# Performance work log

Hardware: AMD Instinct MI355X
Metric: run time of the kernel (lower is better)

Reference implementation:

```python
import jax, jax.numpy as jnp
import numpy as np

NEG_SLOPE = 0.2  # PyG GATConv default negative_slope


def gat_conv(x, edge_index, W, att_src, att_dst, bias):
    # PyG GATConv, heads=1, add_self_loops=True, lin bias=False, final bias added
    N = x.shape[0]
    h = x @ W                                     # [N, F]
    loops = jnp.arange(N, dtype=edge_index.dtype)
    src = jnp.concatenate([edge_index[0], loops])
    dst = jnp.concatenate([edge_index[1], loops])
    a_src = h @ att_src                           # [N]
    a_dst = h @ att_dst                           # [N]
    e = a_src[src] + a_dst[dst]
    e = jnp.where(e > 0, e, NEG_SLOPE * e)        # leaky_relu
    m = jax.ops.segment_max(e, dst, num_segments=N)
    w = jnp.exp(e - m[dst])
    denom = jax.ops.segment_sum(w, dst, num_segments=N)
    alpha = w / denom[dst]
    out = jax.ops.segment_sum(h[src] * alpha[:, None], dst, num_segments=N)
    return out + bias


def gcn_conv(x, edge_index, W, b):
    # PyG GCNConv: add self-loops + symmetric normalization
    N = x.shape[0]
    loops = jnp.arange(N, dtype=edge_index.dtype)
    src = jnp.concatenate([edge_index[0], loops])
    dst = jnp.concatenate([edge_index[1], loops])
    deg = jax.ops.segment_sum(jnp.ones(src.shape[0], dtype=x.dtype), dst, num_segments=N)
    dinv = jax.lax.rsqrt(jnp.maximum(deg, 1e-12))  # deg >= 1 thanks to self-loops
    norm = dinv[src] * dinv[dst]
    xw = x @ W
    return jax.ops.segment_sum(xw[src] * norm[:, None], dst, num_segments=N) + b


def get_final_node(x, batch, num_graphs):
    nn_ = jax.ops.segment_sum(jnp.ones(x.shape[0], dtype=jnp.int32), batch, num_segments=num_graphs)
    cum = jnp.concatenate([jnp.zeros(1, dtype=nn_.dtype), jnp.cumsum(nn_)[:-1]])
    return x[cum]


def ontology_emb(table, e1, e2, W, asrc, adst, b, idx_map):
    emb = gat_conv(table, e1, W, asrc, adst, b)
    emb = gat_conv(emb, e2, W, asrc, adst, b)
    return emb[idx_map]


def _forward(spec_emb, diag_table, proce_table, atc_table,
             diag_W, diag_asrc, diag_adst, diag_b,
             proce_W, proce_asrc, proce_adst, proce_b,
             atc_W, atc_asrc, atc_adst, atc_b,
             gcn_W1, gcn_b1, gcn_W2, gcn_b2, gcn_W3, gcn_b3,
             diag_e1, diag_e2, proce_e1, proce_e2, atc_e1, atc_e2,
             diag_map, proce_map, atc_map,
             left_x, left_graph_index, right_x, right_graph_index,
             left_x_batch, right_x_batch, num_graphs):
    diag_emb = ontology_emb(diag_table, diag_e1, diag_e2, diag_W, diag_asrc, diag_adst, diag_b, diag_map)
    proce_emb = ontology_emb(proce_table, proce_e1, proce_e2, proce_W, proce_asrc, proce_adst, proce_b, proce_map)
    atc_emb = ontology_emb(atc_table, atc_e1, atc_e2, atc_W, atc_asrc, atc_adst, atc_b, atc_map)
    all_emb = jnp.concatenate([spec_emb, diag_emb, proce_emb, atc_emb], axis=0)
    lh = all_emb[left_x[:, 0]]   # squeeze(dim=1)
    rh = all_emb[right_x[:, 0]]
    for W, b in ((gcn_W1, gcn_b1), (gcn_W2, gcn_b2), (gcn_W3, gcn_b3)):
        lh = gcn_conv(lh, left_graph_index, W, b)
        rh = gcn_conv(rh, right_graph_index, W, b)
    lf = get_final_node(lh, left_x_batch, num_graphs)
    rf = get_final_node(rh, right_x_batch, num_graphs)
    eps = 1e-6  # CosineSimilarity eps
    num = jnp.sum(lf * rf, axis=-1)
    den = jnp.maximum(jnp.linalg.norm(lf, axis=-1), eps) * jnp.maximum(jnp.linalg.norm(rf, axis=-1), eps)
    return num / den


def setup_inputs() -> dict:
    key = jax.random.key(0)
    ks = jax.random.split(key, 32)
    HID = 128
    B, NPG = 2048, 50
    N = B * NPG               # 102400 nodes per side
    E_PAT = 409600            # 4 edges per node
    DIAG_N, DIAG_L = 30000, 20000
    PROCE_N, PROCE_L = 12000, 8000
    ATC_N, ATC_L = 6000, 4000
    ALL = 1 + DIAG_L + PROCE_L + ATC_L
    f = lambda k, s: jax.random.normal(k, s, dtype=jnp.float32)
    scale = 0.1
    inp = {
        'spec_emb': f(ks[0], (1, HID)),
        'diag_table': f(ks[1], (DIAG_N, HID)),
        'proce_table': f(ks[2], (PROCE_N, HID)),
        'atc_table': f(ks[3], (ATC_N, HID)),
    }
    for i, nm in enumerate(['diag', 'proce', 'atc']):
        inp[nm + '_W'] = f(ks[4 + i], (HID, HID)) * scale
        inp[nm + '_asrc'] = f(ks[7 + i], (HID,)) * scale
        inp[nm + '_adst'] = f(ks[10 + i], (HID,)) * scale
        inp[nm + '_b'] = jnp.zeros((HID,), jnp.float32)
    for j in range(3):
        inp['gcn_W%d' % (j + 1)] = f(ks[13 + j], (HID, HID)) * scale
        inp['gcn_b%d' % (j + 1)] = jnp.zeros((HID,), jnp.float32)
    inp['diag_e1'] = jax.random.randint(ks[16], (2, DIAG_N), 0, DIAG_N, dtype=jnp.int32)
    inp['diag_e2'] = jax.random.randint(ks[17], (2, DIAG_N), 0, DIAG_N, dtype=jnp.int32)
    inp['proce_e1'] = jax.random.randint(ks[18], (2, PROCE_N), 0, PROCE_N, dtype=jnp.int32)
    inp['proce_e2'] = jax.random.randint(ks[19], (2, PROCE_N), 0, PROCE_N, dtype=jnp.int32)
    inp['atc_e1'] = jax.random.randint(ks[20], (2, ATC_N), 0, ATC_N, dtype=jnp.int32)
    inp['atc_e2'] = jax.random.randint(ks[21], (2, ATC_N), 0, ATC_N, dtype=jnp.int32)
    inp['diag_map'] = jnp.arange(DIAG_L, dtype=jnp.int32)
    inp['proce_map'] = jnp.arange(PROCE_L, dtype=jnp.int32)
    inp['atc_map'] = jnp.arange(ATC_L, dtype=jnp.int32)
    inp['left_x'] = jax.random.randint(ks[22], (N, 1), 0, ALL, dtype=jnp.int32)
    inp['right_x'] = jax.random.randint(ks[23], (N, 1), 0, ALL, dtype=jnp.int32)
    inp['left_graph_index'] = jax.random.randint(ks[24], (2, E_PAT), 0, N, dtype=jnp.int32)
    inp['right_graph_index'] = jax.random.randint(ks[25], (2, E_PAT), 0, N, dtype=jnp.int32)
    batch = jnp.repeat(jnp.arange(B, dtype=jnp.int32), NPG)
    inp['left_x_batch'] = batch
    inp['right_x_batch'] = batch
    inp['num_graphs'] = B
    return inp


def reference(spec_emb, diag_table, proce_table, atc_table,
              diag_W, diag_asrc, diag_adst, diag_b,
              proce_W, proce_asrc, proce_adst, proce_b,
              atc_W, atc_asrc, atc_adst, atc_b,
              gcn_W1, gcn_b1, gcn_W2, gcn_b2, gcn_W3, gcn_b3,
              diag_e1, diag_e2, proce_e1, proce_e2, atc_e1, atc_e2,
              diag_map, proce_map, atc_map,
              left_x, left_graph_index, right_x, right_graph_index,
              left_x_batch, right_x_batch, num_graphs):
    return _forward(spec_emb, diag_table, proce_table, atc_table,
                    diag_W, diag_asrc, diag_adst, diag_b,
                    proce_W, proce_asrc, proce_adst, proce_b,
                    atc_W, atc_asrc, atc_adst, atc_b,
                    gcn_W1, gcn_b1, gcn_W2, gcn_b2, gcn_W3, gcn_b3,
                    diag_e1, diag_e2, proce_e1, proce_e2, atc_e1, atc_e2,
                    diag_map, proce_map, atc_map,
                    left_x, left_graph_index, right_x, right_graph_index,
                    left_x_batch, right_x_batch, num_graphs)
```

## Files before the change

kernel.cpp:

```cpp
#include <hip/hip_runtime.h>
#include <hip/hip_bf16.h>

#define HID 128

typedef unsigned int uint;
typedef unsigned short ushort;
typedef short short8 __attribute__((ext_vector_type(8)));
typedef float f32x4 __attribute__((ext_vector_type(4)));

static inline int cdiv_i(long a, long b) { return (int)((a + b - 1) / b); }

__device__ __forceinline__ float bf2f(uint hi) {
    return __builtin_bit_cast(float, hi << 16);
}
__device__ __forceinline__ ushort f2bf(float f) {
    uint u = __builtin_bit_cast(uint, f);
    u = (u + 0x7fffu + ((u >> 16) & 1u)) >> 16;
    return (ushort)u;
}

__global__ void fold1(const float* __restrict__ W2, const float* __restrict__ b2,
                      const float* __restrict__ W3, float* __restrict__ W23b) {
    const int idx = blockIdx.x * 256 + threadIdx.x;
    if (idx >= 129 * 128) return;
    const int i = idx >> 7, j = idx & 127;
    const float* a = (i < 128) ? (W2 + i * 128) : b2;
    float s = 0.f;
#pragma unroll 8
    for (int k = 0; k < 128; ++k) s += a[k] * W3[k * 128 + j];
    W23b[idx] = s;
}

__global__ void fold2(const float* __restrict__ W1, const float* __restrict__ b1,
                      const float* __restrict__ W23b, float* __restrict__ Pout) {
    const int idx = blockIdx.x * 256 + threadIdx.x;
    if (idx >= 130 * 128) return;
    const int i = idx >> 7, j = idx & 127;
    if (i == 129) { Pout[idx] = W23b[128 * 128 + j]; return; }
    const float* a = (i < 128) ? (W1 + i * 128) : b1;
    float s = 0.f;
#pragma unroll 8
    for (int k = 0; k < 128; ++k) s += a[k] * W23b[k * 128 + j];
    Pout[idx] = s;
}

struct W4 { const float* w[4]; };

__global__ void wtrans_k(W4 ws, ushort* __restrict__ out) {
    const int idx = blockIdx.x * 256 + threadIdx.x;
    if (idx >= 4 * 16384) return;
    const int m = idx >> 14;
    const int e = idx & 16383;
    const int n = e >> 7, k = e & 127;
    out[idx] = f2bf(ws.w[m][k * 128 + n]);
}

__device__ __forceinline__ void stage_wt(const ushort* __restrict__ Wt,
                                         ushort* __restrict__ wl) {
    const int t = threadIdx.x;
    const int row = t >> 1, half = (t & 1) * 64;
    const uint4* src = (const uint4*)(Wt + row * 128 + half);
    uint4* dst = (uint4*)(wl + row * 136 + half);
#pragma unroll
    for (int i = 0; i < 8; ++i) dst[i] = src[i];
}

template <typename AT>
__device__ __forceinline__ void load_afrag(const AT* __restrict__ A, long row,
                                           int koff, short8& af) {
    if constexpr (__is_same(AT, ushort)) {
        const uint4 raw = *(const uint4*)(A + row * 128 + koff);
        af = __builtin_bit_cast(short8, raw);
    } else {
        const float4* p = (const float4*)(A + row * 128 + koff);
        const float4 x0 = p[0], x1 = p[1];
        af[0] = (short)f2bf(x0.x); af[1] = (short)f2bf(x0.y);
        af[2] = (short)f2bf(x0.z); af[3] = (short)f2bf(x0.w);
        af[4] = (short)f2bf(x1.x); af[5] = (short)f2bf(x1.y);
        af[6] = (short)f2bf(x1.z); af[7] = (short)f2bf(x1.w);
    }
}

template <typename AT, typename OT>
__device__ __forceinline__ void mfma_tile(const AT* __restrict__ A,
                                          const ushort* __restrict__ wl,
                                          const float* __restrict__ bias,
                                          OT* __restrict__ C,
                                          long m0blk, long rowEnd) {
    const int tid = threadIdx.x;
    const int wave = tid >> 6, lane = tid & 63;
    const int r = lane & 15, q = lane >> 4;
    const long m0 = m0blk + wave * 32;

    f32x4 acc[2][8];
#pragma unroll
    for (int mi = 0; mi < 2; ++mi)
#pragma unroll
        for (int ni = 0; ni < 8; ++ni) acc[mi][ni] = (f32x4)0.f;

#pragma unroll
    for (int t = 0; t < 4; ++t) {
        const int koff = t * 32 + q * 8;
        short8 bfr[8];
#pragma unroll
        for (int ni = 0; ni < 8; ++ni) {
            const uint4 raw = *(const uint4*)(&wl[(ni * 16 + r) * 136 + koff]);
            bfr[ni] = __builtin_bit_cast(short8, raw);
        }
#pragma unroll
        for (int mi = 0; mi < 2; ++mi) {
            long row = m0 + mi * 16 + r;
            if (row >= rowEnd) row = rowEnd - 1;
            short8 af;
            load_afrag<AT>(A, row, koff, af);
#pragma unroll
            for (int ni = 0; ni < 8; ++ni)
                acc[mi][ni] = __builtin_amdgcn_mfma_f32_16x16x32_bf16(
                    af, bfr[ni], acc[mi][ni], 0, 0, 0);
        }
    }

#pragma unroll
    for (int mi = 0; mi < 2; ++mi) {
#pragma unroll
        for (int ni = 0; ni < 8; ++ni) {
            const int col = ni * 16 + r;
            const float bv = bias ? bias[col] : 0.f;
#pragma unroll
            for (int reg = 0; reg < 4; ++reg) {
                const long row = m0 + mi * 16 + q * 4 + reg;
                if (row < rowEnd) {
                    const float v = acc[mi][ni][reg] + bv;
                    if constexpr (__is_same(OT, ushort))
                        C[row * 128 + col] = f2bf(v);
                    else
                        C[row * 128 + col] = v;
                }
            }
        }
    }
}

template <typename OT>
__global__ __launch_bounds__(256) void gemm_gcn(const ushort* __restrict__ A,
                                                const ushort* __restrict__ Wt,
                                                const float* __restrict__ bias,
                                                OT* __restrict__ C, int M) {
    __shared__ ushort wl[128 * 136];
    stage_wt(Wt, wl);
    __syncthreads();
    const long m0 = (long)blockIdx.x * 256;
    mfma_tile<ushort, OT>(A, wl, bias, C, m0, M);
    if (m0 + 128 < M)
        mfma_tile<ushort, OT>(A, wl, bias, C, m0 + 128, M);
}

struct GOnto {
    const ushort* Wt0; const ushort* Wt1; const ushort* Wt2;
    const float* s0; const float* s1; const float* s2;
    const float* d0; const float* d1; const float* d2;
    int bs1, bs2;
    int r1, r2, r3;
};

template <typename AT>
__global__ __launch_bounds__(256) void gemm_onto(const AT* x0, const AT* x1,
                                                 const AT* x2, GOnto g,
                                                 ushort* __restrict__ H,
                                                 float* __restrict__ as_o,
                                                 float* __restrict__ ad_o) {
    __shared__ ushort wl[128 * 136];
    const int b = blockIdx.x;
    const int gid = (b >= g.bs1) + (b >= g.bs2);
    const ushort* Wt = (gid == 0) ? g.Wt0 : (gid == 1) ? g.Wt1 : g.Wt2;
    const float* avs = (gid == 0) ? g.s0 : (gid == 1) ? g.s1 : g.s2;
    const float* avd = (gid == 0) ? g.d0 : (gid == 1) ? g.d1 : g.d2;
    const AT* Ag = (gid == 0) ? x0 : (gid == 1) ? x1 : x2;
    const int bloc = b - ((gid == 0) ? 0 : (gid == 1) ? g.bs1 : g.bs2);
    const long rb = (gid == 0) ? 0 : (gid == 1) ? g.r1 : g.r2;
    const long Mg = ((gid == 0) ? g.r1 : (gid == 1) ? g.r2 : g.r3) - rb;
    stage_wt(Wt, wl);
    __syncthreads();

    const int tid = threadIdx.x;
    const int wave = tid >> 6, lane = tid & 63;
    const int r = lane & 15, q = lane >> 4;
    const long m0 = (long)bloc * 128 + wave * 32;

    f32x4 acc[2][8];
#pragma unroll
    for (int mi = 0; mi < 2; ++mi)
#pragma unroll
        for (int ni = 0; ni < 8; ++ni) acc[mi][ni] = (f32x4)0.f;

#pragma unroll
// ... 39 lines not shown
        adv[ni] = avd[ni * 16 + r];
    }
#pragma unroll
    for (int mi = 0; mi < 2; ++mi) {
#pragma unroll
        for (int reg = 0; reg < 4; ++reg) {
            float ps = 0.f, pd = 0.f;
#pragma unroll
            for (int ni = 0; ni < 8; ++ni) {
                ps += acc[mi][ni][reg] * asv[ni];
                pd += acc[mi][ni][reg] * adv[ni];
            }
#pragma unroll
            for (int o = 1; o < 16; o <<= 1) {
                ps += __shfl_xor(ps, o);
                pd += __shfl_xor(pd, o);
            }
            const long row = m0 + mi * 16 + q * 4 + reg;
            if (r == 0 && row < Mg) {
                as_o[rb + row] = ps;
                ad_o[rb + row] = pd;
            }
        }
    }
}

struct GatP {
    int r1, r2;
    int ob0, ob1, ob2;
    const float* b0; const float* b1; const float* b2;
};

__device__ __forceinline__ void acc8(float* acc, float w, const uint4 v) {
    acc[0] += w * bf2f(v.x & 0xffff);
    acc[1] += w * bf2f(v.x >> 16);
    acc[2] += w * bf2f(v.y & 0xffff);
    acc[3] += w * bf2f(v.y >> 16);
    acc[4] += w * bf2f(v.z & 0xffff);
    acc[5] += w * bf2f(v.z >> 16);
    acc[6] += w * bf2f(v.w & 0xffff);
    acc[7] += w * bf2f(v.w >> 16);
}

__global__ __launch_bounds__(256) void gat_all(const ushort* __restrict__ h,
                                               const float* __restrict__ as,
                                               const float* __restrict__ ad,
// ... 28 lines not shown
        const uint4 v0 = *(const uint4*)(h + (size_t)(rb + s0) * 128 + ql * 8);
        const uint4 v1 = *(const uint4*)(h + (size_t)(rb + s1) * 128 + ql * 8);
        denom += w0 + w1;
        acc8(acc, w0, v0);
        acc8(acc, w1, v1);
    }
    if (j < end) {
        const int s0 = srcl[j];
        float e0 = as[rb + s0] + adv; e0 = (e0 > 0.f) ? e0 : 0.2f * e0;
        const float w0 = __expf(e0 - m);
        const uint4 v0 = *(const uint4*)(h + (size_t)(rb + s0) * 128 + ql * 8);
        denom += w0;
        acc8(acc, w0, v0);
    }
    const float inv = 1.f / denom;
    const float4 bv0 = *(const float4*)(bias + ql * 8);
    const float4 bv1 = *(const float4*)(bias + ql * 8 + 4);
    uint4 o;
    o.x = (uint)f2bf(acc[0] * inv + bv0.x) | ((uint)f2bf(acc[1] * inv + bv0.y) << 16);
    o.y = (uint)f2bf(acc[2] * inv + bv0.z) | ((uint)f2bf(acc[3] * inv + bv0.w) << 16);
    o.z = (uint)f2bf(acc[4] * inv + bv1.x) | ((uint)f2bf(acc[5] * inv + bv1.y) << 16);
    o.w = (uint)f2bf(acc[6] * inv + bv1.z) | ((uint)f2bf(acc[7] * inv + bv1.w) << 16);
    *(uint4*)(out + (size_t)node * 128 + ql * 8) = o;
}

struct CsrDesc {
    const int* esrc[8];
    const int* edst[8];
    int ebase[9];
    int nbase[9];
    int totE;
};

__global__ void csr_count_b(CsrDesc d, int* __restrict__ cnt, int* __restrict__ pos) {
    const int i = blockIdx.x * 256 + threadIdx.x;
    if (i >= d.totE) return;
    int li = 0;
#pragma unroll
    for (int k = 1; k < 8; ++k) li += (i >= d.ebase[k]);
    const int v = d.nbase[li] + d.edst[li][i - d.ebase[li]];
    pos[i] = atomicAdd(&cnt[v], 1);
}

__global__ void csr_fill_b(CsrDesc d, const int* __restrict__ offs,
                           const int* __restrict__ pos, const int* __restrict__ cnt,
                           int* __restrict__ srcl, int4* __restrict__ pedge,
                           const float* __restrict__ dinv,
                           const int* __restrict__ lx, const int* __restrict__ rx,
                           const int* __restrict__ mk,
                           int NP, int NV, int pB) {
    const int i = blockIdx.x * 256 + threadIdx.x;
    int v, s, li, idx;
    if (i < d.totE) {
        li = 0;
#pragma unroll
        for (int k = 1; k < 8; ++k) li += (i >= d.ebase[k]);
        const int j = i - d.ebase[li];
        v = d.nbase[li] + d.edst[li][j];
        s = d.esrc[li][j];
        idx = offs[v] + pos[i];
    } else if (i < d.totE + NV) {
        v = i - d.totE;
        li = 0;
#pragma unroll
        for (int k = 1; k < 8; ++k) li += (v >= d.nbase[k]);
        s = v - d.nbase[li];
        idx = offs[v] + cnt[v];
    } else return;
    if (li >= 6) {
        const int n2l = v - d.nbase[6];
        if (mk[n2l] == 0) return;
        const int sg = (li - 6) * NP + s;
        int4 rec;
        rec.x = sg;
        rec.y = (li == 7 ? rx : lx)[s];
        rec.z = __float_as_int(dinv[n2l] * dinv[sg]);
        rec.w = 0;
        pedge[idx - pB] = rec;
    } else {
        srcl[idx] = s;
    }
}

__global__ void first_node(const int* __restrict__ bL, const int* __restrict__ bR,
                           int NP, int* __restrict__ gfL, int* __restrict__ gfR,
                           int* __restrict__ mk) {
    const int i = blockIdx.x * 256 + threadIdx.x;
    if (i >= 2 * NP) return;
    const int side = i >= NP;
    const int ii = i - (side ? NP : 0);
    const int* b = side ? bR : bL;
    int* gf = side ? gfR : gfL;
    const int cur = b[ii];
    const int prev = (ii == 0) ? -1 : b[ii - 1];
    if (cur > prev) {
        for (int g = prev + 1; g <= cur; ++g) gf[g] = ii;
        mk[i] = 1;
    }
}

__global__ void mark_k(const int* __restrict__ lEg, const int* __restrict__ rEg,
                       int EP, int NP, int* __restrict__ mk, int testBit, int setBit) {
    const int i = blockIdx.x * 256 + threadIdx.x;
    int src, dst;
    if (i < 2 * EP) {
        const int side = i >= EP;
        const int e = i - side * EP;
        const int* eg = side ? rEg : lEg;
        src = side * NP + eg[e];
        dst = side * NP + eg[EP + e];
    } else if (i < 2 * EP + 2 * NP) {
        src = dst = i - 2 * EP;
    } else return;
    if (mk[dst] & testBit) atomicOr(&mk[src], setBit);
}

__global__ __launch_bounds__(1024) void scan_tile(const int* __restrict__ in,
                                                  int* __restrict__ out,
                                                  int* __restrict__ bsum, int n,
                                                  int pn0, int pcnt,
                                                  float* __restrict__ dinv) {
    __shared__ int buf[1024];
    const int tid = threadIdx.x;
    const int i = blockIdx.x * 1024 + tid;
    const int v = (i < n) ? (in[i] + 1) : 0;
    if (i >= pn0 && i < pn0 + pcnt)
        dinv[i - pn0] = rsqrtf(fmaxf((float)v, 1e-12f));
    buf[tid] = v;
    __syncthreads();
    int x = v;
    for (int o = 1; o < 1024; o <<= 1) {
        const int t = (tid >= o) ? buf[tid - o] : 0;
        __syncthreads();
        x += t;
        buf[tid] = x;
        __syncthreads();
    }
    if (i < n) out[i] = x - v;
    if (tid == 1023) bsum[blockIdx.x] = x;
}

__global__ __launch_bounds__(1024) void scan_single(int* __restrict__ bsum, int nb) {
    __shared__ int buf[1024];
    const int tid = threadIdx.x;
    const int v = (tid < nb) ? bsum[tid] : 0;
    buf[tid] = v;
    __syncthreads();
    int x = v;
    for (int o = 1; o < 1024; o <<= 1) {
        const int t = (tid >= o) ? buf[tid - o] : 0;
        __syncthreads();
        x += t;
        buf[tid] = x;
        __syncthreads();
    }
    if (tid < nb) bsum[tid] = x - v;
    if (tid == 1023) bsum[nb] = x;
}

__global__ void scan_add(int* __restrict__ out, const int* __restrict__ bsum,
                         int n, int nb) {
    const int i = blockIdx.x * 256 + threadIdx.x;
    if (i < n) out[i] += bsum[i >> 10];
    else if (i == n) out[i] = bsum[nb];
}

struct EmbD {
    const float* spec; const ushort* oE;
    const int* m0; const int* m1; const int* m2;
    int lb2, lb3;
    int r1, r2;
    long ALLr;
};

__global__ void build_emb(EmbD d, ushort* __restrict__ out) {
    const long t = (long)blockIdx.x * 256 + threadIdx.x;
    if (t >= d.ALLr * 16) return;
    const int row = (int)(t >> 4), c = (int)(t & 15);
    uint4 o;
    if (row == 0) {
        const float4 f0 = ((const float4*)d.spec)[c * 2];
        const float4 f1 = ((const float4*)d.spec)[c * 2 + 1];
        o.x = (uint)f2bf(f0.x) | ((uint)f2bf(f0.y) << 16);
        o.y = (uint)f2bf(f0.z) | ((uint)f2bf(f0.w) << 16);
        o.z = (uint)f2bf(f1.x) | ((uint)f2bf(f1.y) << 16);
        o.w = (uint)f2bf(f1.z) | ((uint)f2bf(f1.w) << 16);
    } else {
        const int seg = (row >= d.lb2) + (row >= d.lb3);
        const int local = row - ((seg == 0) ? 1 : (seg == 1) ? d.lb2 : d.lb3);
        const int* mp = (seg == 0) ? d.m0 : (seg == 1) ? d.m1 : d.m2;
        const int rb = (seg == 0) ? 0 : (seg == 1) ? d.r1 : d.r2;
        o = ((const uint4*)(d.oE + (size_t)(rb + mp[local]) * 128))[c];
    }
    ((uint4*)out)[(size_t)row * 16 + c] = o;
}

__global__ __launch_bounds__(256) void gcn_agg1(const ushort* __restrict__ A3,
                                                const int4* __restrict__ pedge,
                                                const int* __restrict__ offs6,
                                                const float* __restrict__ c1,
                                                ushort* __restrict__ t1,
                                                const int* __restrict__ mk,
                                                int NP2, int pB) {
    const int n2 = blockIdx.x * 16 + (threadIdx.x >> 4);
    const int ql = threadIdx.x & 15;
    if (n2 >= NP2) return;
    if ((mk[n2] & 4) == 0) return;
    const int beg = offs6[n2] - pB, end = offs6[n2 + 1] - pB;
    float acc[8] = {0.f, 0.f, 0.f, 0.f, 0.f, 0.f, 0.f, 0.f};
    int j = beg;
    for (; j + 2 <= end; j += 2) {
        const int4 r0 = pedge[j], r1 = pedge[j + 1];
        const float w0 = __int_as_float(r0.z), w1 = __int_as_float(r1.z);
        const uint4 v0 = *(const uint4*)(A3 + (size_t)r0.y * 128 + ql * 8);
        const uint4 v1 = *(const uint4*)(A3 + (size_t)r1.y * 128 + ql * 8);
        acc8(acc, w0, v0);
        acc8(acc, w1, v1);
// ... 145 lines not shown
    int nb_acc = 0;
    for (int i = 0; i < 8; ++i) {
        dsc.ebase[i + 1] = dsc.ebase[i] + eCnt[i];
        dsc.nbase[i] = nb_acc;
        nb_acc += nCnt[i];
    }
    const int NV = nb_acc;
    dsc.nbase[8] = NV;
    dsc.totE = dsc.ebase[8];
    const int totEntries = dsc.totE + NV;
    const int pB = dsc.ebase[6] + dsc.nbase[6];
    const int pEntries = totEntries - pB;

    char* ws = (char*)d_ws;
    size_t off = 0;
    auto alloc = [&](size_t bytes) -> void* {
        off = (off + 255) & ~(size_t)255;
        void* p = ws + off;
        off += bytes;
        return p;
    };
    ushort* wt4 = (ushort*)alloc((size_t)4 * 16384 * 2);
    float* W23b = (float*)alloc((size_t)129 * 128 * 4);
    float* Pout = (float*)alloc((size_t)130 * 128 * 4);
    ushort* allemb = (ushort*)alloc((size_t)ALL * HID * 2);
    ushort* A3 = (ushort*)alloc((size_t)ALL * HID * 2);
    int* cnt = (int*)alloc((size_t)NV * 4);
    int* offs = (int*)alloc((size_t)(NV + 1) * 4);
    int* pos = (int*)alloc((size_t)dsc.totE * 4);
    int* srcl = (int*)alloc((size_t)pB * 4);
    int4* pedge = (int4*)alloc((size_t)pEntries * 16);
    int* bsum = (int*)alloc(1025 * 4);
    float* dinv = (float*)alloc((size_t)2 * NP * 4);
    float* as = (float*)alloc((size_t)Mtot * 4);
    float* ad = (float*)alloc((size_t)Mtot * 4);
    int* gfL = (int*)alloc((size_t)(B + 1) * 4);
    int* gfR = (int*)alloc((size_t)(B + 1) * 4);
    int* mk = (int*)alloc((size_t)2 * NP * 4);
    ushort* t1 = (ushort*)alloc((size_t)2 * NP * HID * 2);
    ushort* big = (ushort*)alloc((size_t)2 * NP * HID * 2);
    ushort* hbuf = big;
    ushort* obuf = big + (size_t)Mtot * HID;
    ushort* t2 = big;

    fold1<<<cdiv_i(129 * 128, 256), 256, 0, stream>>>(gcnW[1], gcnB[1], gcnW[2], W23b);
    fold2<<<cdiv_i(130 * 128, 256), 256, 0, stream>>>(gcnW[0], gcnB[0], W23b, Pout);
    const float* c1 = Pout + 128 * 128;
    const float* c2 = Pout + 129 * 128;

    W4 w4;
    w4.w[0] = ontW[0]; w4.w[1] = ontW[1]; w4.w[2] = ontW[2]; w4.w[3] = Pout;
    wtrans_k<<<cdiv_i(4 * 16384, 256), 256, 0, stream>>>(w4, wt4);
    const ushort* wtOnt[3] = {wt4, wt4 + 16384, wt4 + 2 * 16384};
    const ushort* WpT = wt4 + 3 * 16384;

    hipMemsetAsync(mk, 0, (size_t)2 * NP * 4, stream);
    first_node<<<cdiv_i(2 * NP, 256), 256, 0, stream>>>(left_batch, right_batch,
                                                        NP, gfL, gfR, mk);
    mark_k<<<cdiv_i(2 * EP + 2 * NP, 256), 256, 0, stream>>>(
        left_eg, right_eg, EP, NP, mk, 1, 2);
    mark_k<<<cdiv_i(2 * EP + 2 * NP, 256), 256, 0, stream>>>(
        left_eg, right_eg, EP, NP, mk, 2, 4);

    hipMemsetAsync(cnt, 0, (size_t)NV * 4, stream);
    csr_count_b<<<cdiv_i(dsc.totE, 256), 256, 0, stream>>>(dsc, cnt, pos);
    {
        const int nb = cdiv_i(NV, 1024);
        scan_tile<<<nb, 1024, 0, stream>>>(cnt, offs, bsum, NV, dsc.nbase[6],
                                           2 * NP, dinv);
        scan_single<<<1, 1024, 0, stream>>>(bsum, nb);
        scan_add<<<cdiv_i(NV + 1, 256), 256, 0, stream>>>(offs, bsum, NV, nb);
    }
    csr_fill_b<<<cdiv_i(totEntries, 256), 256, 0, stream>>>(dsc, offs, pos, cnt,
                                                            srcl, pedge, dinv,
                                                            left_x, right_x, mk,
                                                            NP, NV, pB);

    GOnto go;
    go.Wt0 = wtOnt[0]; go.Wt1 = wtOnt[1]; go.Wt2 = wtOnt[2];
    go.s0 = ontAs[0]; go.s1 = ontAs[1]; go.s2 = ontAs[2];
    go.d0 = ontAd[0]; go.d1 = ontAd[1]; go.d2 = ontAd[2];
    go.bs1 = cdiv_i(Ms[0], 128);
    go.bs2 = go.bs1 + cdiv_i(Ms[1], 128);
    const int totBlk = go.bs2 + cdiv_i(Ms[2], 128);
    go.r1 = r1; go.r2 = r2; go.r3 = Mtot;

    for (int layer = 0; layer < 2; ++layer) {
        const GatP gp{r1, r2,
                      dsc.nbase[0 + layer], dsc.nbase[2 + layer], dsc.nbase[4 + layer],
                      ontB[0], ontB[1], ontB[2]};
        if (layer == 0)
            gemm_onto<float><<<totBlk, 256, 0, stream>>>(tabs[0], tabs[1], tabs[2],
                                                         go, hbuf, as, ad);
        else
            gemm_onto<ushort><<<totBlk, 256, 0, stream>>>(
                obuf, obuf + (size_t)r1 * HID, obuf + (size_t)r2 * HID,
                go, hbuf, as, ad);
        gat_all<<<cdiv_i(Mtot, 16), 256, 0, stream>>>(hbuf, as, ad, offs, srcl, gp,
                                                      obuf, Mtot);
    }

    EmbD ed;
    ed.spec = spec; ed.oE = obuf;
    ed.m0 = maps[0]; ed.m1 = maps[1]; ed.m2 = maps[2];
    ed.lb2 = 1 + Ls[0]; ed.lb3 = 1 + Ls[0] + Ls[1];
    ed.r1 = r1; ed.r2 = r2; ed.ALLr = ALL;
    build_emb<<<cdiv_i(ALL * 16, 256), 256, 0, stream>>>(ed, allemb);

    const int* offs6 = offs + dsc.nbase[6];
    gemm_gcn<ushort><<<cdiv_i(ALL, 256), 256, 0, stream>>>(
        allemb, WpT, nullptr, A3, (int)ALL);
    gcn_agg1<<<cdiv_i(2 * NP, 16), 256, 0, stream>>>(A3, pedge, offs6, c1, t1,
                                                     mk, 2 * NP, pB);
    gcn_agg2<<<cdiv_i(2 * NP, 16), 256, 0, stream>>>(t1, pedge, offs6, c2, t2,
                                                     mk, 2 * NP, pB);
    final_cos<<<cdiv_i(B, 8), 256, 0, stream>>>(t2, pedge, offs6, gfL, gfR,
                                                gcnB[2], (float*)d_out, B, NP, pB);
}
```

Baseline: 396.1 us.

## Fuse preprocessing kernels into packed launches and gather embeddings inside GEMM

Independent setup kernels (weight folding, transposes, memsets, first-node, CSR count, mark passes, layer-1 GEMM) are merged into a few multi-role launches that dispatch on block index. The three-kernel scan becomes two kernels. The embedding build is folded into the patient GEMM's A-fragment load, and fold2 writes the transposed bf16 weight directly. This removes many launch gaps and an intermediate buffer round trip, at the cost of heterogeneous blocks sharing one launch and padding shared-memory use onto blocks that never need it.

```diff
diff --git a/kernel.cpp b/kernel.cpp
--- a/kernel.cpp
+++ b/kernel.cpp
@@ -9,6 +9,7 @@
 typedef float f32x4 __attribute__((ext_vector_type(4)));
 
 static inline int cdiv_i(long a, long b) { return (int)((a + b - 1) / b); }
+static inline int imax_i(int a, int b) { return a > b ? a : b; }
 
 __device__ __forceinline__ float bf2f(uint hi) {
     return __builtin_bit_cast(float, hi << 16);
@@ -19,41 +20,13 @@
     return (ushort)u;
 }
 
-__global__ void fold1(const float* __restrict__ W2, const float* __restrict__ b2,
-                      const float* __restrict__ W3, float* __restrict__ W23b) {
-    const int idx = blockIdx.x * 256 + threadIdx.x;
-    if (idx >= 129 * 128) return;
-    const int i = idx >> 7, j = idx & 127;
-    const float* a = (i < 128) ? (W2 + i * 128) : b2;
-    float s = 0.f;
-#pragma unroll 8
-    for (int k = 0; k < 128; ++k) s += a[k] * W3[k * 128 + j];
-    W23b[idx] = s;
-}
-
-__global__ void fold2(const float* __restrict__ W1, const float* __restrict__ b1,
-                      const float* __restrict__ W23b, float* __restrict__ Pout) {
-    const int idx = blockIdx.x * 256 + threadIdx.x;
-    if (idx >= 130 * 128) return;
-    const int i = idx >> 7, j = idx & 127;
-    if (i == 129) { Pout[idx] = W23b[128 * 128 + j]; return; }
-    const float* a = (i < 128) ? (W1 + i * 128) : b1;
-    float s = 0.f;
-#pragma unroll 8
-    for (int k = 0; k < 128; ++k) s += a[k] * W23b[k * 128 + j];
-    Pout[idx] = s;
-}
-
-struct W4 { const float* w[4]; };
-
-__global__ void wtrans_k(W4 ws, ushort* __restrict__ out) {
-    const int idx = blockIdx.x * 256 + threadIdx.x;
-    if (idx >= 4 * 16384) return;
-    const int m = idx >> 14;
-    const int e = idx & 16383;
-    const int n = e >> 7, k = e & 127;
-    out[idx] = f2bf(ws.w[m][k * 128 + n]);
-}
+struct CsrDesc {
+    const int* esrc[8];
+    const int* edst[8];
+    int ebase[9];
+    int nbase[9];
+    int totE;
+};
 
 __device__ __forceinline__ void stage_wt(const ushort* __restrict__ Wt,
                                          ushort* __restrict__ wl) {
@@ -81,80 +54,6 @@
     }
 }
 
-template <typename AT, typename OT>
-__device__ __forceinline__ void mfma_tile(const AT* __restrict__ A,
-                                          const ushort* __restrict__ wl,
-                                          const float* __restrict__ bias,
-                                          OT* __restrict__ C,
-                                          long m0blk, long rowEnd) {
-    const int tid = threadIdx.x;
-    const int wave = tid >> 6, lane = tid & 63;
-    const int r = lane & 15, q = lane >> 4;
-    const long m0 = m0blk + wave * 32;
-
-    f32x4 acc[2][8];
-#pragma unroll
-    for (int mi = 0; mi < 2; ++mi)
-#pragma unroll
-        for (int ni = 0; ni < 8; ++ni) acc[mi][ni] = (f32x4)0.f;
-
-#pragma unroll
-    for (int t = 0; t < 4; ++t) {
-        const int koff = t * 32 + q * 8;
-        short8 bfr[8];
-#pragma unroll
-        for (int ni = 0; ni < 8; ++ni) {
-            const uint4 raw = *(const uint4*)(&wl[(ni * 16 + r) * 136 + koff]);
-            bfr[ni] = __builtin_bit_cast(short8, raw);
-        }
-#pragma unroll
-        for (int mi = 0; mi < 2; ++mi) {
-            long row = m0 + mi * 16 + r;
-            if (row >= rowEnd) row = rowEnd - 1;
-            short8 af;
-            load_afrag<AT>(A, row, koff, af);
-#pragma unroll
-            for (int ni = 0; ni < 8; ++ni)
-                acc[mi][ni] = __builtin_amdgcn_mfma_f32_16x16x32_bf16(
-                    af, bfr[ni], acc[mi][ni], 0, 0, 0);
-        }
-    }
-
-#pragma unroll
-    for (int mi = 0; mi < 2; ++mi) {
-#pragma unroll
-        for (int ni = 0; ni < 8; ++ni) {
-            const int col = ni * 16 + r;
-            const float bv = bias ? bias[col] : 0.f;
-#pragma unroll
-            for (int reg = 0; reg < 4; ++reg) {
-                const long row = m0 + mi * 16 + q * 4 + reg;
-                if (row < rowEnd) {
-                    const float v = acc[mi][ni][reg] + bv;
-                    if constexpr (__is_same(OT, ushort))
-                        C[row * 128 + col] = f2bf(v);
-                    else
-                        C[row * 128 + col] = v;
-                }
-            }
-        }
-    }
-}
-
-template <typename OT>
-__global__ __launch_bounds__(256) void gemm_gcn(const ushort* __restrict__ A,
-                                                const ushort* __restrict__ Wt,
-                                                const float* __restrict__ bias,
-                                                OT* __restrict__ C, int M) {
-    __shared__ ushort wl[128 * 136];
-    stage_wt(Wt, wl);
-    __syncthreads();
-    const long m0 = (long)blockIdx.x * 256;
-    mfma_tile<ushort, OT>(A, wl, bias, C, m0, M);
-    if (m0 + 128 < M)
-        mfma_tile<ushort, OT>(A, wl, bias, C, m0 + 128, M);
-}
-
 struct GOnto {
     const ushort* Wt0; const ushort* Wt1; const ushort* Wt2;
     const float* s0; const float* s1; const float* s2;
@@ -164,13 +63,11 @@
 };
 
 template <typename AT>
-__global__ __launch_bounds__(256) void gemm_onto(const AT* x0, const AT* x1,
-                                                 const AT* x2, GOnto g,
-                                                 ushort* __restrict__ H,
-                                                 float* __restrict__ as_o,
-                                                 float* __restrict__ ad_o) {
-    __shared__ ushort wl[128 * 136];
-    const int b = blockIdx.x;
+__device__ void gemm_onto_dev(int b, const AT* __restrict__ x0,
+                              const AT* __restrict__ x1, const AT* __restrict__ x2,
+                              const GOnto& g, ushort* __restrict__ H,
+                              float* __restrict__ as_o, float* __restrict__ ad_o,
+                              ushort* __restrict__ wl) {
     const int gid = (b >= g.bs1) + (b >= g.bs2);
     const ushort* Wt = (gid == 0) ? g.Wt0 : (gid == 1) ? g.Wt1 : g.Wt2;
     const float* avs = (gid == 0) ? g.s0 : (gid == 1) ? g.s1 : g.s2;
@@ -256,6 +153,342 @@
                 ad_o[rb + row] = pd;
             }
         }
+    }
+}
+
+__global__ __launch_bounds__(256) void gemm_onto_l2(const ushort* __restrict__ x0,
+                                                    const ushort* __restrict__ x1,
+                                                    const ushort* __restrict__ x2,
+                                                    GOnto g, ushort* __restrict__ H,
+                                                    float* __restrict__ as_o,
+                                                    float* __restrict__ ad_o) {
+    __shared__ ushort wl[128 * 136];
+    gemm_onto_dev<ushort>(blockIdx.x, x0, x1, x2, g, H, as_o, ad_o, wl);
+}
+
+struct EmbSrc {
+    const float* spec; const ushort* oE;
+    const int* m0; const int* m1; const int* m2;
+    int lb2, lb3, r1, r2;
+};
+
+__device__ __forceinline__ short8 load_emb(const EmbSrc& e, long row, int koff) {
+    short8 af;
+    if (row == 0) {
+        const float4* pp = (const float4*)(e.spec + koff);
+        const float4 x0 = pp[0], x1 = pp[1];
+        af[0] = (short)f2bf(x0.x); af[1] = (short)f2bf(x0.y);
+        af[2] = (short)f2bf(x0.z); af[3] = (short)f2bf(x0.w);
+        af[4] = (short)f2bf(x1.x); af[5] = (short)f2bf(x1.y);
+        af[6] = (short)f2bf(x1.z); af[7] = (short)f2bf(x1.w);
+        return af;
+    }
+    const int r = (int)row;
+    const int seg = (r >= e.lb2) + (r >= e.lb3);
+    const int local = r - ((seg == 0) ? 1 : (seg == 1) ? e.lb2 : e.lb3);
+    const int* mp = (seg == 0) ? e.m0 : (seg == 1) ? e.m1 : e.m2;
+    const int rb = (seg == 0) ? 0 : (seg == 1) ? e.r1 : e.r2;
+    const long sr = (long)rb + mp[local];
+    return __builtin_bit_cast(short8, *(const uint4*)(e.oE + sr * 128 + koff));
+}
+
+__device__ void gemm_pat_tile(const EmbSrc& es, const ushort* __restrict__ wl,
+                              ushort* __restrict__ C, long m0blk, long rowEnd) {
+    const int tid = threadIdx.x;
+    const int wave = tid >> 6, lane = tid & 63;
+    const int r = lane & 15, q = lane >> 4;
+    const long m0 = m0blk + wave * 32;
+
+    f32x4 acc[2][8];
+#pragma unroll
+    for (int mi = 0; mi < 2; ++mi)
+#pragma unroll
+        for (int ni = 0; ni < 8; ++ni) acc[mi][ni] = (f32x4)0.f;
+
+#pragma unroll
+    for (int t = 0; t < 4; ++t) {
+        const int koff = t * 32 + q * 8;
+        short8 bfr[8];
+#pragma unroll
+        for (int ni = 0; ni < 8; ++ni) {
+            const uint4 raw = *(const uint4*)(&wl[(ni * 16 + r) * 136 + koff]);
+            bfr[ni] = __builtin_bit_cast(short8, raw);
+        }
+#pragma unroll
+        for (int mi = 0; mi < 2; ++mi) {
+            long row = m0 + mi * 16 + r;
+            if (row >= rowEnd) row = rowEnd - 1;
+            const short8 af = load_emb(es, row, koff);
+#pragma unroll
+            for (int ni = 0; ni < 8; ++ni)
+                acc[mi][ni] = __builtin_amdgcn_mfma_f32_16x16x32_bf16(
+                    af, bfr[ni], acc[mi][ni], 0, 0, 0);
+        }
+    }
+
+#pragma unroll
+    for (int mi = 0; mi < 2; ++mi) {
+#pragma unroll
+        for (int ni = 0; ni < 8; ++ni) {
+            const int col = ni * 16 + r;
+#pragma unroll
+            for (int reg = 0; reg < 4; ++reg) {
+                const long row = m0 + mi * 16 + q * 4 + reg;
+                if (row < rowEnd) C[row * 128 + col] = f2bf(acc[mi][ni][reg]);
+            }
+        }
+    }
+}
+
+__global__ __launch_bounds__(256) void gemm_pat(EmbSrc es,
+                                                const ushort* __restrict__ Wt,
+                                                ushort* __restrict__ C, int M) {
+    __shared__ ushort wl[128 * 136];
+    stage_wt(Wt, wl);
+    __syncthreads();
+    const long m0 = (long)blockIdx.x * 256;
+    gemm_pat_tile(es, wl, C, m0, M);
+    if (m0 + 128 < M) gemm_pat_tile(es, wl, C, m0 + 128, M);
+}
+
+__device__ __forceinline__ void fold1_dev(int idx, const float* __restrict__ W2,
+                                          const float* __restrict__ b2,
+                                          const float* __restrict__ W3,
+                                          float* __restrict__ W23b) {
+    if (idx >= 129 * 128) return;
+    const int i = idx >> 7, j = idx & 127;
+    const float* a = (i < 128) ? (W2 + i * 128) : b2;
+    float s = 0.f;
+#pragma unroll 8
+    for (int k = 0; k < 128; ++k) s += a[k] * W3[k * 128 + j];
+    W23b[idx] = s;
+}
+
+__device__ __forceinline__ void fold2_dev(int idx, const float* __restrict__ W1,
+                                          const float* __restrict__ b1,
+                                          const float* __restrict__ W23b,
+                                          ushort* __restrict__ WpT,
+                                          float* __restrict__ cbuf) {
+    if (idx >= 130 * 128) return;
+    const int i = idx >> 7, j = idx & 127;
+    if (i == 129) { cbuf[128 + j] = W23b[128 * 128 + j]; return; }
+    const float* a = (i < 128) ? (W1 + i * 128) : b1;
+    float s = 0.f;
+#pragma unroll 8
+    for (int k = 0; k < 128; ++k) s += a[k] * W23b[k * 128 + j];
+    if (i < 128) WpT[j * 128 + i] = f2bf(s);
+    else cbuf[j] = s;
+}
+
+__device__ __forceinline__ void mark_dev(int i, const int* __restrict__ lEg,
+                                         const int* __restrict__ rEg, int EP,
+                                         int NP, int* __restrict__ mk,
+                                         int testBit, int setBit) {
+    int src, dst;
+    if (i < 2 * EP) {
+        const int side = i >= EP;
+        const int e = i - side * EP;
+        const int* eg = side ? rEg : lEg;
+        src = side * NP + eg[e];
+        dst = side * NP + eg[EP + e];
+    } else if (i < 2 * EP + 2 * NP) {
+        src = dst = i - 2 * EP;
+    } else return;
+    if (mk[dst] & testBit) atomicOr(&mk[src], setBit);
+}
+
+__device__ __forceinline__ void csr_count_dev(int i, const CsrDesc& d,
+                                              int* __restrict__ cnt,
+                                              int* __restrict__ pos) {
+    if (i >= d.totE) return;
+    int li = 0;
+#pragma unroll
+    for (int k = 1; k < 8; ++k) li += (i >= d.ebase[k]);
+    const int v = d.nbase[li] + d.edst[li][i - d.ebase[li]];
+    pos[i] = atomicAdd(&cnt[v], 1);
+}
+
+struct PackPrep {
+    const float* W2; const float* b2; const float* W3; float* W23b;
+    const float* wsrc[3]; ushort* wt_out;
+    int* cnt; int NV;
+    const int* bL; const int* bR; int NP;
+    int* gfL; int* gfR; int* mk;
+    int nbF1, nbWT, nbInit;
+};
+
+__global__ __launch_bounds__(256) void k_prep(PackPrep p) {
+    const int b = blockIdx.x, tid = threadIdx.x;
+    if (b < p.nbF1) {
+        fold1_dev(b * 256 + tid, p.W2, p.b2, p.W3, p.W23b);
+    } else if (b < p.nbF1 + p.nbWT) {
+        const int idx = (b - p.nbF1) * 256 + tid;
+        if (idx < 3 * 16384) {
+            const int m = idx >> 14;
+            const int e = idx & 16383;
+            const int n = e >> 7, k = e & 127;
+            p.wt_out[idx] = f2bf(p.wsrc[m][k * 128 + n]);
+        }
+    } else {
+        const int i = (b - p.nbF1 - p.nbWT) * 256 + tid;
+        if (i < p.NV) p.cnt[i] = 0;
+        if (i < 2 * p.NP) {
+            const int side = i >= p.NP;
+            const int ii = i - (side ? p.NP : 0);
+            const int* bb = side ? p.bR : p.bL;
+            int* gf = side ? p.gfR : p.gfL;
+            const int cur = bb[ii];
+            const int prev = (ii == 0) ? -1 : bb[ii - 1];
+            int m = 0;
+            if (cur > prev) {
+                for (int g = prev + 1; g <= cur; ++g) gf[g] = ii;
+                m = 1;
+            }
+            p.mk[i] = m;
+        }
+    }
+}
+
+struct PackA {
+    const float* W1; const float* b1; const float* W23b;
+    ushort* WpT; float* cbuf;
+    CsrDesc dsc; int* cnt; int* pos;
+    const int* lEg; const int* rEg; int EP; int NP; int* mk;
+    const float* x0; const float* x1; const float* x2;
+    GOnto go; ushort* H; float* as_o; float* ad_o;
+    int nbF2, nbCnt, nbMark;
+};
+
+__global__ __launch_bounds__(256) void k_packA(PackA p) {
+    __shared__ ushort wl[128 * 136];
+    const int b = blockIdx.x, tid = threadIdx.x;
+    if (b < p.nbF2) {
+        fold2_dev(b * 256 + tid, p.W1, p.b1, p.W23b, p.WpT, p.cbuf);
+    } else if (b < p.nbF2 + p.nbCnt) {
+        csr_count_dev((b - p.nbF2) * 256 + tid, p.dsc, p.cnt, p.pos);
+    } else if (b < p.nbF2 + p.nbCnt + p.nbMark) {
+        mark_dev((b - p.nbF2 - p.nbCnt) * 256 + tid, p.lEg, p.rEg, p.EP, p.NP,
+                 p.mk, 1, 2);
+    } else {
+        gemm_onto_dev<float>(b - p.nbF2 - p.nbCnt - p.nbMark, p.x0, p.x1, p.x2,
+                             p.go, p.H, p.as_o, p.ad_o, wl);
+    }
+}
+
+struct PackB {
+    const int* cnt; int* offs; int* bsum;
+    int NV; int pn0; int pcnt; float* dinv;
+    const int* lEg; const int* rEg; int EP; int NP; int* mk;
+    int nbScan;
+};
+
+__device__ void scan_tile_dev(const int* __restrict__ in, int* __restrict__ out,
+                              int* __restrict__ bsum, int n, int pn0, int pcnt,
+                              float* __restrict__ dinv, int tb, int tid,
+                              int* sbuf) {
+    const int base = tb * 1024 + tid * 4;
+    int v[4];
+    int s = 0;
+#pragma unroll
+    for (int k = 0; k < 4; ++k) {
+        const int i = base + k;
+        v[k] = (i < n) ? (in[i] + 1) : 0;
+        if (i >= pn0 && i < pn0 + pcnt)
+            dinv[i - pn0] = rsqrtf(fmaxf((float)v[k], 1e-12f));
+        s += v[k];
+    }
+    sbuf[tid] = s;
+    __syncthreads();
+    int x = s;
+    for (int o = 1; o < 256; o <<= 1) {
+        const int t = (tid >= o) ? sbuf[tid - o] : 0;
+        __syncthreads();
+        x += t;
+        sbuf[tid] = x;
+        __syncthreads();
+    }
+    int run = x - s;
+#pragma unroll
+    for (int k = 0; k < 4; ++k) {
+        const int i = base + k;
+        if (i < n) out[i] = run;
+        run += v[k];
+    }
+    if (tid == 255) bsum[tb] = x;
+}
+
+__global__ __launch_bounds__(256) void k_packB(PackB p) {
+    __shared__ int sbuf[256];
+    const int b = blockIdx.x, tid = threadIdx.x;
+    if (b < p.nbScan) {
+        scan_tile_dev(p.cnt, p.offs, p.bsum, p.NV, p.pn0, p.pcnt, p.dinv, b,
+                      tid, sbuf);
+    } else {
+        mark_dev((b - p.nbScan) * 256 + tid, p.lEg, p.rEg, p.EP, p.NP, p.mk, 2, 4);
+    }
+}
+
+__global__ __launch_bounds__(256) void k_scanfin(int* __restrict__ out,
+                                                 const int* __restrict__ bsum,
+                                                 int n, int nbData) {
+    __shared__ int sbuf[256];
+    const int tb = blockIdx.x, tid = threadIdx.x;
+    int pLim = tb < nbData ? tb : nbData;
+    int pth = 0;
+    for (int j = tid; j < pLim; j += 256) pth += bsum[j];
+    sbuf[tid] = pth;
+    __syncthreads();
+    for (int o = 128; o > 0; o >>= 1) {
+        if (tid < o) sbuf[tid] += sbuf[tid + o];
+        __syncthreads();
+    }
+    const int prefix = sbuf[0];
+    const int base = tb * 1024 + tid * 4;
+#pragma unroll
+    for (int k = 0; k < 4; ++k) {
+        const int i = base + k;
+        if (i < n) out[i] += prefix;
+        else if (i == n) out[i] = prefix + ((tb < nbData) ? bsum[tb] : 0);
+    }
+}
+
+__global__ void csr_fill_b(CsrDesc d, const int* __restrict__ offs,
+                           const int* __restrict__ pos, const int* __restrict__ cnt,
+                           int* __restrict__ srcl, int4* __restrict__ pedge,
+                           const float* __restrict__ dinv,
+                           const int* __restrict__ lx, const int* __restrict__ rx,
+                           const int* __restrict__ mk,
+                           int NP, int NV, int pB) {
+    const int i = blockIdx.x * 256 + threadIdx.x;
+    int v, s, li, idx;
+    if (i < d.totE) {
+        li = 0;
+#pragma unroll
+        for (int k = 1; k < 8; ++k) li += (i >= d.ebase[k]);
+        const int j = i - d.ebase[li];
+        v = d.nbase[li] + d.edst[li][j];
+        s = d.esrc[li][j];
+        idx = offs[v] + pos[i];
+    } else if (i < d.totE + NV) {
+        v = i - d.totE;
+        li = 0;
+#pragma unroll
+        for (int k = 1; k < 8; ++k) li += (v >= d.nbase[k]);
+        s = v - d.nbase[li];
+        idx = offs[v] + cnt[v];
+    } else return;
+    if (li >= 6) {
+        const int n2l = v - d.nbase[6];
+        if (mk[n2l] == 0) return;
+        const int sg = (li - 6) * NP + s;
+        int4 rec;
+        rec.x = sg;
+        rec.y = (li == 7 ? rx : lx)[s];
+        rec.z = __float_as_int(dinv[n2l] * dinv[sg]);
+        rec.w = 0;
+        pedge[idx - pB] = rec;
+    } else {
+        srcl[idx] = s;
     }
 }
 
@@ -330,177 +563,6 @@
     o.z = (uint)f2bf(acc[4] * inv + bv1.x) | ((uint)f2bf(acc[5] * inv + bv1.y) << 16);
     o.w = (uint)f2bf(acc[6] * inv + bv1.z) | ((uint)f2bf(acc[7] * inv + bv1.w) << 16);
     *(uint4*)(out + (size_t)node * 128 + ql * 8) = o;
-}
-
-struct CsrDesc {
-    const int* esrc[8];
-    const int* edst[8];
-    int ebase[9];
-    int nbase[9];
-    int totE;
-};
-
-__global__ void csr_count_b(CsrDesc d, int* __restrict__ cnt, int* __restrict__ pos) {
-    const int i = blockIdx.x * 256 + threadIdx.x;
-    if (i >= d.totE) return;
-    int li = 0;
-#pragma unroll
-    for (int k = 1; k < 8; ++k) li += (i >= d.ebase[k]);
-    const int v = d.nbase[li] + d.edst[li][i - d.ebase[li]];
-    pos[i] = atomicAdd(&cnt[v], 1);
-}
-
-__global__ void csr_fill_b(CsrDesc d, const int* __restrict__ offs,
-                           const int* __restrict__ pos, const int* __restrict__ cnt,
-                           int* __restrict__ srcl, int4* __restrict__ pedge,
-                           const float* __restrict__ dinv,
-                           const int* __restrict__ lx, const int* __restrict__ rx,
-                           const int* __restrict__ mk,
-                           int NP, int NV, int pB) {
-    const int i = blockIdx.x * 256 + threadIdx.x;
-    int v, s, li, idx;
-    if (i < d.totE) {
-        li = 0;
-#pragma unroll
-        for (int k = 1; k < 8; ++k) li += (i >= d.ebase[k]);
-        const int j = i - d.ebase[li];
-        v = d.nbase[li] + d.edst[li][j];
-        s = d.esrc[li][j];
-        idx = offs[v] + pos[i];
-    } else if (i < d.totE + NV) {
-        v = i - d.totE;
-        li = 0;
-#pragma unroll
-        for (int k = 1; k < 8; ++k) li += (v >= d.nbase[k]);
-        s = v - d.nbase[li];
-        idx = offs[v] + cnt[v];
-    } else return;
-    if (li >= 6) {
-        const int n2l = v - d.nbase[6];
-        if (mk[n2l] == 0) return;
-        const int sg = (li - 6) * NP + s;
-        int4 rec;
-        rec.x = sg;
-        rec.y = (li == 7 ? rx : lx)[s];
-        rec.z = __float_as_int(dinv[n2l] * dinv[sg]);
-        rec.w = 0;
-        pedge[idx - pB] = rec;
-    } else {
-        srcl[idx] = s;
-    }
-}
-
-__global__ void first_node(const int* __restrict__ bL, const int* __restrict__ bR,
-                           int NP, int* __restrict__ gfL, int* __restrict__ gfR,
-                           int* __restrict__ mk) {
-    const int i = blockIdx.x * 256 + threadIdx.x;
-    if (i >= 2 * NP) return;
-    const int side = i >= NP;
-    const int ii = i - (side ? NP : 0);
-    const int* b = side ? bR : bL;
-    int* gf = side ? gfR : gfL;
-    const int cur = b[ii];
-    const int prev = (ii == 0) ? -1 : b[ii - 1];
-    if (cur > prev) {
-        for (int g = prev + 1; g <= cur; ++g) gf[g] = ii;
-        mk[i] = 1;
-    }
-}
-
-__global__ void mark_k(const int* __restrict__ lEg, const int* __restrict__ rEg,
-                       int EP, int NP, int* __restrict__ mk, int testBit, int setBit) {
-    const int i = blockIdx.x * 256 + threadIdx.x;
-    int src, dst;
-    if (i < 2 * EP) {
-        const int side = i >= EP;
-        const int e = i - side * EP;
-        const int* eg = side ? rEg : lEg;
-        src = side * NP + eg[e];
-        dst = side * NP + eg[EP + e];
-    } else if (i < 2 * EP + 2 * NP) {
-        src = dst = i - 2 * EP;
-    } else return;
-    if (mk[dst] & testBit) atomicOr(&mk[src], setBit);
-}
-
-__global__ __launch_bounds__(1024) void scan_tile(const int* __restrict__ in,
-                                                  int* __restrict__ out,
-                                                  int* __restrict__ bsum, int n,
-                                                  int pn0, int pcnt,
-                                                  float* __restrict__ dinv) {
-    __shared__ int buf[1024];
-    const int tid = threadIdx.x;
-    const int i = blockIdx.x * 1024 + tid;
-    const int v = (i < n) ? (in[i] + 1) : 0;
-    if (i >= pn0 && i < pn0 + pcnt)
-        dinv[i - pn0] = rsqrtf(fmaxf((float)v, 1e-12f));
-    buf[tid] = v;
-    __syncthreads();
-    int x = v;
-    for (int o = 1; o < 1024; o <<= 1) {
-        const int t = (tid >= o) ? buf[tid - o] : 0;
-        __syncthreads();
-        x += t;
-        buf[tid] = x;
-        __syncthreads();
-    }
-    if (i < n) out[i] = x - v;
-    if (tid == 1023) bsum[blockIdx.x] = x;
-}
-
-__global__ __launch_bounds__(1024) void scan_single(int* __restrict__ bsum, int nb) {
-    __shared__ int buf[1024];
-    const int tid = threadIdx.x;
-    const int v = (tid < nb) ? bsum[tid] : 0;
-    buf[tid] = v;
-    __syncthreads();
-    int x = v;
-    for (int o = 1; o < 1024; o <<= 1) {
-        const int t = (tid >= o) ? buf[tid - o] : 0;
-        __syncthreads();
-        x += t;
-        buf[tid] = x;
-        __syncthreads();
-    }
-    if (tid < nb) bsum[tid] = x - v;
-    if (tid == 1023) bsum[nb] = x;
-}
-
-__global__ void scan_add(int* __restrict__ out, const int* __restrict__ bsum,
-                         int n, int nb) {
-    const int i = blockIdx.x * 256 + threadIdx.x;
-    if (i < n) out[i] += bsum[i >> 10];
-    else if (i == n) out[i] = bsum[nb];
-}
-
-struct EmbD {
-    const float* spec; const ushort* oE;
-    const int* m0; const int* m1; const int* m2;
-    int lb2, lb3;
-    int r1, r2;
-    long ALLr;
-};
-
-__global__ void build_emb(EmbD d, ushort* __restrict__ out) {
-    const long t = (long)blockIdx.x * 256 + threadIdx.x;
-    if (t >= d.ALLr * 16) return;
-    const int row = (int)(t >> 4), c = (int)(t & 15);
-    uint4 o;
-    if (row == 0) {
-        const float4 f0 = ((const float4*)d.spec)[c * 2];
-        const float4 f1 = ((const float4*)d.spec)[c * 2 + 1];
-        o.x = (uint)f2bf(f0.x) | ((uint)f2bf(f0.y) << 16);
-        o.y = (uint)f2bf(f0.z) | ((uint)f2bf(f0.w) << 16);
-        o.z = (uint)f2bf(f1.x) | ((uint)f2bf(f1.y) << 16);
-        o.w = (uint)f2bf(f1.z) | ((uint)f2bf(f1.w) << 16);
-    } else {
-        const int seg = (row >= d.lb2) + (row >= d.lb3);
-        const int local = row - ((seg == 0) ? 1 : (seg == 1) ? d.lb2 : d.lb3);
-        const int* mp = (seg == 0) ? d.m0 : (seg == 1) ? d.m1 : d.m2;
-        const int rb = (seg == 0) ? 0 : (seg == 1) ? d.r1 : d.r2;
-        o = ((const uint4*)(d.oE + (size_t)(rb + mp[local]) * 128))[c];
-    }
-    ((uint4*)out)[(size_t)row * 16 + c] = o;
 }
 
 __global__ __launch_bounds__(256) void gcn_agg1(const ushort* __restrict__ A3,
@@ -692,8 +754,7 @@
     };
     ushort* wt4 = (ushort*)alloc((size_t)4 * 16384 * 2);
     float* W23b = (float*)alloc((size_t)129 * 128 * 4);
-    float* Pout = (float*)alloc((size_t)130 * 128 * 4);
-    ushort* allemb = (ushort*)alloc((size_t)ALL * HID * 2);
+    float* cbuf = (float*)alloc((size_t)256 * 4);
     ushort* A3 = (ushort*)alloc((size_t)ALL * HID * 2);
     int* cnt = (int*)alloc((size_t)NV * 4);
     int* offs = (int*)alloc((size_t)(NV + 1) * 4);
@@ -713,38 +774,22 @@
     ushort* obuf = big + (size_t)Mtot * HID;
     ushort* t2 = big;
 
-    fold1<<<cdiv_i(129 * 128, 256), 256, 0, stream>>>(gcnW[1], gcnB[1], gcnW[2], W23b);
-    fold2<<<cdiv_i(130 * 128, 256), 256, 0, stream>>>(gcnW[0], gcnB[0], W23b, Pout);
-    const float* c1 = Pout + 128 * 128;
-    const float* c2 = Pout + 129 * 128;
-
-    W4 w4;
-    w4.w[0] = ontW[0]; w4.w[1] = ontW[1]; w4.w[2] = ontW[2]; w4.w[3] = Pout;
-    wtrans_k<<<cdiv_i(4 * 16384, 256), 256, 0, stream>>>(w4, wt4);
     const ushort* wtOnt[3] = {wt4, wt4 + 16384, wt4 + 2 * 16384};
-    const ushort* WpT = wt4 + 3 * 16384;
-
-    hipMemsetAsync(mk, 0, (size_t)2 * NP * 4, stream);
-    first_node<<<cdiv_i(2 * NP, 256), 256, 0, stream>>>(left_batch, right_batch,
-                                                        NP, gfL, gfR, mk);
-    mark_k<<<cdiv_i(2 * EP + 2 * NP, 256), 256, 0, stream>>>(
-        left_eg, right_eg, EP, NP, mk, 1, 2);
-    mark_k<<<cdiv_i(2 * EP + 2 * NP, 256), 256, 0, stream>>>(
-        left_eg, right_eg, EP, NP, mk, 2, 4);
-
-    hipMemsetAsync(cnt, 0, (size_t)NV * 4, stream);
-    csr_count_b<<<cdiv_i(dsc.totE, 256), 256, 0, stream>>>(dsc, cnt, pos);
-    {
-        const int nb = cdiv_i(NV, 1024);
-        scan_tile<<<nb, 1024, 0, stream>>>(cnt, offs, bsum, NV, dsc.nbase[6],
-                                           2 * NP, dinv);
-        scan_single<<<1, 1024, 0, stream>>>(bsum, nb);
-        scan_add<<<cdiv_i(NV + 1, 256), 256, 0, stream>>>(offs, bsum, NV, nb);
-    }
-    csr_fill_b<<<cdiv_i(totEntries, 256), 256, 0, stream>>>(dsc, offs, pos, cnt,
-                                                            srcl, pedge, dinv,
-                                                            left_x, right_x, mk,
-                                                            NP, NV, pB);
+    ushort* WpT = wt4 + 3 * 16384;
+    const float* c1 = cbuf;
+    const float* c2 = cbuf + 128;
+
+    PackPrep pp;
+    pp.W2 = gcnW[1]; pp.b2 = gcnB[1]; pp.W3 = gcnW[2]; pp.W23b = W23b;
+    pp.wsrc[0] = ontW[0]; pp.wsrc[1] = ontW[1]; pp.wsrc[2] = ontW[2];
+    pp.wt_out = wt4;
+    pp.cnt = cnt; pp.NV = NV;
+    pp.bL = left_batch; pp.bR = right_batch; pp.NP = NP;
+    pp.gfL = gfL; pp.gfR = gfR; pp.mk = mk;
+    pp.nbF1 = cdiv_i(129 * 128, 256);
+    pp.nbWT = cdiv_i(3 * 16384, 256);
+    pp.nbInit = cdiv_i(imax_i(NV, 2 * NP), 256);
+    k_prep<<<pp.nbF1 + pp.nbWT + pp.nbInit, 256, 0, stream>>>(pp);
 
     GOnto go;
     go.Wt0 = wtOnt[0]; go.Wt1 = wtOnt[1]; go.Wt2 = wtOnt[2];
@@ -755,31 +800,52 @@
     const int totBlk = go.bs2 + cdiv_i(Ms[2], 128);
     go.r1 = r1; go.r2 = r2; go.r3 = Mtot;
 
-    for (int layer = 0; layer < 2; ++layer) {
-        const GatP gp{r1, r2,
-                      dsc.nbase[0 + layer], dsc.nbase[2 + layer], dsc.nbase[4 + layer],
-                      ontB[0], ontB[1], ontB[2]};
-        if (layer == 0)
-            gemm_onto<float><<<totBlk, 256, 0, stream>>>(tabs[0], tabs[1], tabs[2],
-                                                         go, hbuf, as, ad);
-        else
-            gemm_onto<ushort><<<totBlk, 256, 0, stream>>>(
-                obuf, obuf + (size_t)r1 * HID, obuf + (size_t)r2 * HID,
-                go, hbuf, as, ad);
-        gat_all<<<cdiv_i(Mtot, 16), 256, 0, stream>>>(hbuf, as, ad, offs, srcl, gp,
-                                                      obuf, Mtot);
-    }
-
-    EmbD ed;
-    ed.spec = spec; ed.oE = obuf;
-    ed.m0 = maps[0]; ed.m1 = maps[1]; ed.m2 = maps[2];
-    ed.lb2 = 1 + Ls[0]; ed.lb3 = 1 + Ls[0] + Ls[1];
-    ed.r1 = r1; ed.r2 = r2; ed.ALLr = ALL;
-    build_emb<<<cdiv_i(ALL * 16, 256), 256, 0, stream>>>(ed, allemb);
+    PackA pa;
+    pa.W1 = gcnW[0]; pa.b1 = gcnB[0]; pa.W23b = W23b;
+    pa.WpT = WpT; pa.cbuf = cbuf;
+    pa.dsc = dsc; pa.cnt = cnt; pa.pos = pos;
+    pa.lEg = left_eg; pa.rEg = right_eg; pa.EP = EP; pa.NP = NP; pa.mk = mk;
+    pa.x0 = tabs[0]; pa.x1 = tabs[1]; pa.x2 = tabs[2];
+    pa.go = go; pa.H = hbuf; pa.as_o = as; pa.ad_o = ad;
+    pa.nbF2 = cdiv_i(130 * 128, 256);
+    pa.nbCnt = cdiv_i(dsc.totE, 256);
+    pa.nbMark = cdiv_i(2 * EP + 2 * NP, 256);
+    k_packA<<<pa.nbF2 + pa.nbCnt + pa.nbMark + totBlk, 256, 0, stream>>>(pa);
+
+    PackB pb;
+    pb.cnt = cnt; pb.offs = offs; pb.bsum = bsum;
+    pb.NV = NV; pb.pn0 = dsc.nbase[6]; pb.pcnt = 2 * NP; pb.dinv = dinv;
+    pb.lEg = left_eg; pb.rEg = right_eg; pb.EP = EP; pb.NP = NP; pb.mk = mk;
+    pb.nbScan = cdiv_i(NV, 1024);
+    k_packB<<<pb.nbScan + pa.nbMark, 256, 0, stream>>>(pb);
+
+    k_scanfin<<<cdiv_i(NV + 1, 1024), 256, 0, stream>>>(offs, bsum, NV, pb.nbScan);
+
+    csr_fill_b<<<cdiv_i(totEntries, 256), 256, 0, stream>>>(dsc, offs, pos, cnt,
+                                                            srcl, pedge, dinv,
+                                                            left_x, right_x, mk,
+                                                            NP, NV, pB);
+
+    const GatP gp0{r1, r2, dsc.nbase[0], dsc.nbase[2], dsc.nbase[4],
+                   ontB[0], ontB[1], ontB[2]};
+    gat_all<<<cdiv_i(Mtot, 16), 256, 0, stream>>>(hbuf, as, ad, offs, srcl, gp0,
+                                                  obuf, Mtot);
+    gemm_onto_l2<<<totBlk, 256, 0, stream>>>(obuf, obuf + (size_t)r1 * HID,
+                                             obuf + (size_t)r2 * HID, go, hbuf,
+                                             as, ad);
+    const GatP gp1{r1, r2, dsc.nbase[1], dsc.nbase[3], dsc.nbase[5],
+                   ontB[0], ontB[1], ontB[2]};
+    gat_all<<<cdiv_i(Mtot, 16), 256, 0, stream>>>(hbuf, as, ad, offs, srcl, gp1,
+                                                  obuf, Mtot);
+
+    EmbSrc es;
+    es.spec = spec; es.oE = obuf;
+    es.m0 = maps[0]; es.m1 = maps[1]; es.m2 = maps[2];
+    es.lb2 = 1 + Ls[0]; es.lb3 = 1 + Ls[0] + Ls[1];
+    es.r1 = r1; es.r2 = r2;
+    gemm_pat<<<cdiv_i(ALL, 256), 256, 0, stream>>>(es, WpT, A3, (int)ALL);
 
     const int* offs6 = offs + dsc.nbase[6];
-    gemm_gcn<ushort><<<cdiv_i(ALL, 256), 256, 0, stream>>>(
-        allemb, WpT, nullptr, A3, (int)ALL);
     gcn_agg1<<<cdiv_i(2 * NP, 16), 256, 0, stream>>>(A3, pedge, offs6, c1, t1,
                                                      mk, 2 * NP, pB);
     gcn_agg2<<<cdiv_i(2 * NP, 16), 256, 0, stream>>>(t1, pedge, offs6, c2, t2,
```

Result: faster. 361.4 us (-8.8%).
